# Kernel tuning notes

Measured on AMD Instinct MI355X. Metric: run time of the kernel, lower is better.

## Reference

```python
import jax, jax.numpy as jnp
import numpy as np

# Constants from mode='only_tv': gamma_l1=gamma_dwt=beta=lambda_l1=lambda_dwt=sigma=0,
# so u_l1,u_dwt,z,eta_l1,eta_dwt,rho stay identically zero and drop out of the math.
GAMMA_TV = 2.0
ALPHA = 5.0
LAMBDA_TV = 1e-4
N_ITER = 200


def soft_thresh(v, t):
    return jnp.sign(v) * jnp.maximum(jnp.abs(v) - t, 0.0)


def setup_inputs() -> dict:
    key = jax.random.key(0)
    k1, k2, k3 = jax.random.split(key, 3)
    target = jax.random.normal(k1, (4096, 64), dtype=jnp.float32)  # B spectra of K bands
    A = jax.random.normal(k2, (9, 64), dtype=jnp.float32) * 0.1     # (M=9 channels, K=64 bands)
    x0 = jax.random.normal(k3, (4096, 64), dtype=jnp.float32)       # replaces randn_like(target)
    return {"target": target, "A": A, "x0": x0}


def reference(target, A, x0):
    # target, x0: (B, K) batch of per-sample length-K vectors; A: (M, K)
    K = A.shape[1]
    AT = A.T  # (K, M)
    I = jnp.eye(K, dtype=A.dtype)
    Delta = jnp.roll(I, 1, axis=1) - I          # (K, K)
    DtD = Delta.T @ Delta
    inv_item = jnp.linalg.inv(AT @ A + GAMMA_TV * DtD + ALPHA * I)  # (K, K)

    # b = A @ x  per sample  ->  (B, M);  AT @ b per sample -> (B, K)
    b = target @ A.T
    ATb = b @ A

    # per-sample Delta @ v, batched over rows -> v_mat @ Delta.T
    def D(v):
        return v @ Delta.T

    eta_tv0 = jnp.zeros_like(x0)
    tau0 = jnp.zeros_like(x0)

    def step(carry, _):
        x, eta_tv, tau = carry
        u_tv = soft_thresh(D(x) + eta_tv / GAMMA_TV, LAMBDA_TV / GAMMA_TV)
        w = jnp.maximum(x + tau / ALPHA, 0.0)
        # note: torch's matmul(z_tv, DeltaT) on a vector equals Delta @ z_tv -> batched D(.)
        resid = ATb + D(GAMMA_TV * u_tv - eta_tv) + ALPHA * w - tau
        x = resid @ inv_item.T  # per-sample inv_item @ resid
        eta_tv = eta_tv + GAMMA_TV * (D(x) - u_tv)
        tau = tau + ALPHA * (x - w)
        return (x, eta_tv, tau), None

    (x, _, _), _ = jax.lax.scan(step, (x0, eta_tv0, tau0), None, length=N_ITER)
    return x
```

## Files before the change

kernel.cpp:

```cpp
#include <hip/hip_runtime.h>

#define NSAMP 4096
#define NITER 200

typedef float v2f __attribute__((ext_vector_type(2)));

__global__ __launch_bounds__(256) void setup_woodbury(const float* __restrict__ A,
                                                      float* __restrict__ inv_out) {
  __shared__ double lamr[64];
  __shared__ float binv[64];
  __shared__ float P[9][64];
  __shared__ float Q[9][64];
  __shared__ double W[9][18];
  const int tid = threadIdx.x;
  const double TWO_PI = 6.283185307179586476925286766559;

  double cb = 0.0;
  if (tid < 64) {
    cb = cos(TWO_PI * (double)tid / 64.0);
    lamr[tid] = 1.0 / (9.0 - 4.0 * cb);
  }
  __syncthreads();
  if (tid < 64) {
    double cm1 = 1.0, c0 = cb;
    double acc = lamr[0] + cb * lamr[1];
#pragma unroll 16
    for (int m = 2; m < 64; ++m) {
      double c = 2.0 * cb * c0 - cm1;
      cm1 = c0;
      c0 = c;
      acc += c * lamr[m];
    }
    binv[tid] = (float)(acc / 64.0);
  }
  __syncthreads();

  for (int e = tid; e < 9 * 64; e += 256) {
    int m = e >> 6, i = e & 63;
    double acc = 0.0;
#pragma unroll 16
    for (int k = 0; k < 64; ++k)
      acc += (double)A[m * 64 + k] * (double)binv[(k - i) & 63];
    P[m][i] = (float)acc;
  }
  __syncthreads();

  if (tid < 81) {
    int m = tid / 9, n = tid % 9;
    double acc = (m == n) ? 1.0 : 0.0;
#pragma unroll 16
    for (int i = 0; i < 64; ++i)
      acc += (double)P[m][i] * (double)A[n * 64 + i];
    W[m][n] = acc;
    W[m][n + 9] = (m == n) ? 1.0 : 0.0;
  }
  __syncthreads();

  {
    const int r9 = tid / 18, c9 = tid % 18;
    const bool act = (tid < 162);
    for (int k = 0; k < 9; ++k) {
      double pv = 1.0, f = 0.0, wkc = 0.0;
      if (act) {
        pv = W[k][k];
        f = W[r9][k];
        wkc = W[k][c9];
      }
      __syncthreads();
      if (act) {
        double nk = wkc / pv;
        W[r9][c9] = (r9 == k) ? nk : fma(-f, nk, W[r9][c9]);
      }
      __syncthreads();
    }
  }

  for (int e = tid; e < 9 * 64; e += 256) {
    int m = e >> 6, j = e & 63;
    double acc = 0.0;
#pragma unroll
    for (int n = 0; n < 9; ++n) acc += W[m][n + 9] * (double)P[n][j];
    Q[m][j] = (float)acc;
  }
  __syncthreads();

  for (int e = tid; e < 64 * 64; e += 256) {
    int i = e >> 6, j = e & 63;
    float acc = binv[(i - j) & 63];
#pragma unroll
    for (int m = 0; m < 9; ++m) acc = fmaf(-P[m][i], Q[m][j], acc);
    inv_out[e] = acc;
  }
}

__global__ __launch_bounds__(256) __attribute__((amdgpu_waves_per_eu(4, 4)))
void admm_kernel(const float* __restrict__ target, const float* __restrict__ A,
                 const float* __restrict__ x0, const float* __restrict__ invmat,
                 float* __restrict__ out) {
  __shared__ __align__(16) float rbuf[4][64];
  const int tid = threadIdx.x;
  const int wid = tid >> 6;
  const int lane = tid & 63;
  const int s = blockIdx.x * 4 + wid;

  float t = target[s * 64 + lane];
  float atb = 0.f;
#pragma unroll
  for (int m = 0; m < 9; ++m) {
    float a = A[m * 64 + lane];
    float p = t * a;
#pragma unroll
    for (int off = 32; off; off >>= 1) p += __shfl_xor(p, off, 64);
    atb = fmaf(a, p, atb);
  }

  const float* mrow = invmat + lane * 64;
#define LOADM(i) v2f m##i = *reinterpret_cast<const v2f*>(mrow + 2 * (i)); \
                 asm("" : "+v"(m##i))
  LOADM(0);  LOADM(1);  LOADM(2);  LOADM(3);  LOADM(4);  LOADM(5);
  LOADM(6);  LOADM(7);  LOADM(8);  LOADM(9);  LOADM(10); LOADM(11);
  LOADM(12); LOADM(13); LOADM(14); LOADM(15); LOADM(16); LOADM(17);
  LOADM(18); LOADM(19); LOADM(20); LOADM(21); LOADM(22); LOADM(23);
  LOADM(24); LOADM(25); LOADM(26); LOADM(27); LOADM(28); LOADM(29);
  LOADM(30); LOADM(31);
#undef LOADM

  float* rb = &rbuf[wid][0];
  float x = x0[s * 64 + lane];
  float eta = 0.f, tau = 0.f;
  const int nxt = (lane + 1) & 63;
  float Dx = __shfl(x, nxt, 64) - x;

#pragma unroll 1
  for (int it = 0; it < NITER; ++it) {
    float v = fmaf(eta, 0.5f, Dx);
    float u = copysignf(fmaxf(fabsf(v) - 5e-5f, 0.f), v);
    float w = fmaxf(fmaf(tau, 0.2f, x), 0.f);
    float tv = fmaf(2.f, u, -eta);
    float ts = __shfl(tv, nxt, 64);
    float resid = fmaf(5.f, w, atb) + (ts - tv) - tau;

    rb[lane] = resid;
    __builtin_amdgcn_wave_barrier();

    v2f a0 = {0.f, 0.f}, a1 = {0.f, 0.f}, a2 = {0.f, 0.f}, a3 = {0.f, 0.f};
#define STEP2(j, accA, accB, mA, mB)                                        \
    {                                                                       \
      float4 r4 = *reinterpret_cast<const float4*>(rb + 4 * (j));           \
      v2f rlo = {r4.x, r4.y};                                               \
      v2f rhi = {r4.z, r4.w};                                               \
      asm("v_pk_fma_f32 %0, %1, %2, %0" : "+v"(accA) : "v"(mA), "v"(rlo));  \
      asm("v_pk_fma_f32 %0, %1, %2, %0" : "+v"(accB) : "v"(mB), "v"(rhi));  \
    }
    STEP2(0,  a0, a1, m0,  m1);
    STEP2(1,  a2, a3, m2,  m3);
    STEP2(2,  a0, a1, m4,  m5);
    STEP2(3,  a2, a3, m6,  m7);
    STEP2(4,  a0, a1, m8,  m9);
    STEP2(5,  a2, a3, m10, m11);
    STEP2(6,  a0, a1, m12, m13);
    STEP2(7,  a2, a3, m14, m15);
    STEP2(8,  a0, a1, m16, m17);
    STEP2(9,  a2, a3, m18, m19);
    STEP2(10, a0, a1, m20, m21);
    STEP2(11, a2, a3, m22, m23);
    STEP2(12, a0, a1, m24, m25);
    STEP2(13, a2, a3, m26, m27);
    STEP2(14, a0, a1, m28, m29);
    STEP2(15, a2, a3, m30, m31);
#undef STEP2
    __builtin_amdgcn_wave_barrier();
    float xn = ((a0.x + a0.y) + (a1.x + a1.y)) + ((a2.x + a2.y) + (a3.x + a3.y));

    float xs2 = __shfl(xn, nxt, 64);
    Dx = xs2 - xn;
    eta = fmaf(2.f, Dx - u, eta);
    tau = fmaf(5.f, xn - w, tau);
    x = xn;
  }

  out[s * 64 + lane] = x;
}

extern "C" void kernel_launch(void* const* d_in, const int* in_sizes, int n_in,
                              void* d_out, int out_size, void* d_ws, size_t ws_size,
                              hipStream_t stream) {
  const float* target = (const float*)d_in[0];
  const float* A = (const float*)d_in[1];
  const float* x0 = (const float*)d_in[2];
  float* out = (float*)d_out;
  float* inv_ws = (float*)d_ws;

  setup_woodbury<<<1, 256, 0, stream>>>(A, inv_ws);
  admm_kernel<<<NSAMP / 4, 256, 0, stream>>>(target, A, x0, inv_ws, out);
}
```

Baseline: 211.5 us.

## Split each sample's matvec across two waves with shared-memory partial-sum exchange

Each sample is now handled by a pair of waves, each holding half the inverse-matrix columns in registers and computing a half-length dot product per iteration. Partial sums are exchanged through a double-buffered shared array with a block barrier each iteration, and the grid doubles. This shortens the per-wave FMA dependency chain and raises the wave count to fill SIMDs, at the cost of a per-iteration __syncthreads and duplicated elementwise work. The fixed waves-per-EU attribute is dropped.

```diff
diff --git a/kernel.cpp b/kernel.cpp
--- a/kernel.cpp
+++ b/kernel.cpp
@@ -93,15 +93,18 @@
   }
 }
 
-__global__ __launch_bounds__(256) __attribute__((amdgpu_waves_per_eu(4, 4)))
+__global__ __launch_bounds__(256)
 void admm_kernel(const float* __restrict__ target, const float* __restrict__ A,
                  const float* __restrict__ x0, const float* __restrict__ invmat,
                  float* __restrict__ out) {
   __shared__ __align__(16) float rbuf[4][64];
+  __shared__ float pbuf[2][4][64];
   const int tid = threadIdx.x;
   const int wid = tid >> 6;
   const int lane = tid & 63;
-  const int s = blockIdx.x * 4 + wid;
+  const int pairI = wid >> 1;
+  const int half = wid & 1;
+  const int s = blockIdx.x * 2 + pairI;
 
   float t = target[s * 64 + lane];
   float atb = 0.f;
@@ -114,18 +117,20 @@
     atb = fmaf(a, p, atb);
   }
 
-  const float* mrow = invmat + lane * 64;
-#define LOADM(i) v2f m##i = *reinterpret_cast<const v2f*>(mrow + 2 * (i)); \
-                 asm("" : "+v"(m##i))
-  LOADM(0);  LOADM(1);  LOADM(2);  LOADM(3);  LOADM(4);  LOADM(5);
-  LOADM(6);  LOADM(7);  LOADM(8);  LOADM(9);  LOADM(10); LOADM(11);
-  LOADM(12); LOADM(13); LOADM(14); LOADM(15); LOADM(16); LOADM(17);
-  LOADM(18); LOADM(19); LOADM(20); LOADM(21); LOADM(22); LOADM(23);
-  LOADM(24); LOADM(25); LOADM(26); LOADM(27); LOADM(28); LOADM(29);
-  LOADM(30); LOADM(31);
-#undef LOADM
+  const float* mrow = invmat + lane * 64 + half * 32;
+  v2f m0, m1, m2, m3, m4, m5, m6, m7, m8, m9, m10, m11, m12, m13, m14, m15;
+#define LOADQ(q, ma, mb)                                              \
+  {                                                                   \
+    float4 v = reinterpret_cast<const float4*>(mrow)[q];              \
+    ma = (v2f){v.x, v.y};                                             \
+    mb = (v2f){v.z, v.w};                                             \
+  }
+  LOADQ(0, m0, m1) LOADQ(1, m2, m3) LOADQ(2, m4, m5) LOADQ(3, m6, m7)
+  LOADQ(4, m8, m9) LOADQ(5, m10, m11) LOADQ(6, m12, m13) LOADQ(7, m14, m15)
+#undef LOADQ
 
   float* rb = &rbuf[wid][0];
+  const float* rhalf = &rbuf[wid][half * 32];
   float x = x0[s * 64 + lane];
   float eta = 0.f, tau = 0.f;
   const int nxt = (lane + 1) & 63;
@@ -143,34 +148,25 @@
     rb[lane] = resid;
     __builtin_amdgcn_wave_barrier();
 
-    v2f a0 = {0.f, 0.f}, a1 = {0.f, 0.f}, a2 = {0.f, 0.f}, a3 = {0.f, 0.f};
-#define STEP2(j, accA, accB, mA, mB)                                        \
+    v2f a0 = {0.f, 0.f}, a1 = {0.f, 0.f};
+#define STEP2(j, mA, mB)                                                    \
     {                                                                       \
-      float4 r4 = *reinterpret_cast<const float4*>(rb + 4 * (j));           \
+      float4 r4 = *reinterpret_cast<const float4*>(rhalf + 4 * (j));        \
       v2f rlo = {r4.x, r4.y};                                               \
       v2f rhi = {r4.z, r4.w};                                               \
-      asm("v_pk_fma_f32 %0, %1, %2, %0" : "+v"(accA) : "v"(mA), "v"(rlo));  \
-      asm("v_pk_fma_f32 %0, %1, %2, %0" : "+v"(accB) : "v"(mB), "v"(rhi));  \
+      asm("v_pk_fma_f32 %0, %1, %2, %0" : "+v"(a0) : "v"(mA), "v"(rlo));    \
+      asm("v_pk_fma_f32 %0, %1, %2, %0" : "+v"(a1) : "v"(mB), "v"(rhi));    \
     }
-    STEP2(0,  a0, a1, m0,  m1);
-    STEP2(1,  a2, a3, m2,  m3);
-    STEP2(2,  a0, a1, m4,  m5);
-    STEP2(3,  a2, a3, m6,  m7);
-    STEP2(4,  a0, a1, m8,  m9);
-    STEP2(5,  a2, a3, m10, m11);
-    STEP2(6,  a0, a1, m12, m13);
-    STEP2(7,  a2, a3, m14, m15);
-    STEP2(8,  a0, a1, m16, m17);
-    STEP2(9,  a2, a3, m18, m19);
-    STEP2(10, a0, a1, m20, m21);
-    STEP2(11, a2, a3, m22, m23);
-    STEP2(12, a0, a1, m24, m25);
-    STEP2(13, a2, a3, m26, m27);
-    STEP2(14, a0, a1, m28, m29);
-    STEP2(15, a2, a3, m30, m31);
+    STEP2(0, m0, m1)  STEP2(1, m2, m3)  STEP2(2, m4, m5)  STEP2(3, m6, m7)
+    STEP2(4, m8, m9)  STEP2(5, m10, m11) STEP2(6, m12, m13) STEP2(7, m14, m15)
 #undef STEP2
-    __builtin_amdgcn_wave_barrier();
-    float xn = ((a0.x + a0.y) + (a1.x + a1.y)) + ((a2.x + a2.y) + (a3.x + a3.y));
+    float p = (a0.x + a0.y) + (a1.x + a1.y);
+
+    const int par = it & 1;
+    pbuf[par][wid][lane] = p;
+    __syncthreads();
+    float po = pbuf[par][wid ^ 1][lane];
+    float xn = p + po;
 
     float xs2 = __shfl(xn, nxt, 64);
     Dx = xs2 - xn;
@@ -179,7 +175,7 @@
     x = xn;
   }
 
-  out[s * 64 + lane] = x;
+  if (half == 0) out[s * 64 + lane] = x;
 }
 
 extern "C" void kernel_launch(void* const* d_in, const int* in_sizes, int n_in,
@@ -192,5 +188,5 @@
   float* inv_ws = (float*)d_ws;
 
   setup_woodbury<<<1, 256, 0, stream>>>(A, inv_ws);
-  admm_kernel<<<NSAMP / 4, 256, 0, stream>>>(target, A, x0, inv_ws, out);
+  admm_kernel<<<NSAMP / 2, 256, 0, stream>>>(target, A, x0, inv_ws, out);
 }
```

Result: slower. 249.9 us (+18.1%).
